# Kernel optimization log

Hardware: AMD Instinct MI355X
Metric: run time of the kernel (lower is better)

## Reference

```python
import jax, jax.numpy as jnp
import numpy as np

N_NODES = 100000
EPS = 1e-5  # BatchNorm1d default eps


def gcn_conv(x, W, b, row, col, n):
    """PyG GCNConv: add self-loops, symmetric normalization, linear, scatter-add."""
    loop = jnp.arange(n, dtype=row.dtype)
    row_f = jnp.concatenate([row, loop])  # sources
    col_f = jnp.concatenate([col, loop])  # targets
    # degree of target nodes (edge_weight = 1)
    deg = jax.ops.segment_sum(jnp.ones_like(col_f, dtype=x.dtype), col_f, num_segments=n)
    dinv = jnp.where(deg > 0, jax.lax.rsqrt(deg), 0.0)
    norm = dinv[row_f] * dinv[col_f]  # [E+N]
    h = x @ W  # [N, out]
    msg = h[row_f] * norm[:, None]  # [E+N, out]
    out = jax.ops.segment_sum(msg, col_f, num_segments=n)
    return out + b


def batch_norm(x, gamma, beta):
    # training-mode BatchNorm1d: biased batch stats over node axis
    mean = jnp.mean(x, axis=0)
    var = jnp.var(x, axis=0)
    return (x - mean) * jax.lax.rsqrt(var + EPS) * gamma + beta


def setup_inputs() -> dict:
    key = jax.random.key(0)
    ks = jax.random.split(key, 8)
    n, e, f_in, h = N_NODES, 1600000, 25, 128
    x = jax.random.normal(ks[0], (n, f_in), dtype=jnp.float32)
    edge_index = jax.random.randint(ks[1], (2, e), 0, n, dtype=jnp.int64)
    s1 = 1.0 / np.sqrt(f_in)
    s2 = 1.0 / np.sqrt(h)
    W1 = jax.random.uniform(ks[2], (f_in, h), jnp.float32, -s1, s1)
    b1 = jax.random.uniform(ks[3], (h,), jnp.float32, -s1, s1)
    gamma = jnp.ones((h,), jnp.float32)
    beta = jnp.zeros((h,), jnp.float32)
    W2 = jax.random.uniform(ks[4], (h, h), jnp.float32, -s2, s2)
    b2 = jax.random.uniform(ks[5], (h,), jnp.float32, -s2, s2)
    return {"x": x, "edge_index": edge_index, "W1": W1, "b1": b1,
            "gamma": gamma, "beta": beta, "W2": W2, "b2": b2}


def reference(x, edge_index, W1, b1, gamma, beta, W2, b2):
    row, col = edge_index[0], edge_index[1]
    n = x.shape[0]
    h = jax.nn.relu(gcn_conv(x, W1, b1, row, col, n))
    h = batch_norm(h, gamma, beta)
    h = jax.nn.relu(gcn_conv(h, W2, b2, row, col, n))
    return h
```

## Files before the change

kernel.cpp:

```cpp
#include <hip/hip_runtime.h>
#include <stdint.h>


#define HID 128
#define NBB 512

typedef short bf16x8 __attribute__((ext_vector_type(8)));
typedef float f32x4 __attribute__((ext_vector_type(4)));

__device__ __forceinline__ unsigned short f2bf(float f) {
    unsigned int u = __float_as_uint(f);
    unsigned int r = (u + 0x7FFFu + ((u >> 16) & 1u)) >> 16;
    return (unsigned short)r;
}
__device__ __forceinline__ unsigned int pack2bf(float lo, float hi) {
    return (unsigned int)f2bf(lo) | ((unsigned int)f2bf(hi) << 16);
}
__device__ __forceinline__ float bflo(unsigned int v) { return __uint_as_float(v << 16); }
__device__ __forceinline__ float bfhi(unsigned int v) { return __uint_as_float(v & 0xffff0000u); }

__global__ void detect_kernel(const unsigned int* __restrict__ w, int* __restrict__ mode, int nwords) {
    __shared__ int any;
    if (threadIdx.x == 0) any = 0;
    __syncthreads();
    for (int i = threadIdx.x * 2 + 1; i < nwords && i < 8192; i += 512) {
        if (w[i] != 0) atomicOr(&any, 1);
    }
    __syncthreads();
    if (threadIdx.x == 0) *mode = any ? 0 : 1;
}

__device__ __forceinline__ int load_idx(const void* ei, size_t i, int mode) {
    return mode ? (int)((const long long*)ei)[i] : ((const int*)ei)[i];
}

__global__ __launch_bounds__(256) void count_q_kernel(const void* __restrict__ ei,
                                                      const int* __restrict__ modep,
                                                      int* __restrict__ qcnt,
                                                      int E, int CHUNK, int nchunk) {
    __shared__ int qc[512];
    for (int i = threadIdx.x; i < nchunk; i += 256) qc[i] = 0;
    __syncthreads();
    int mode = *modep;
    int beg = blockIdx.x * CHUNK;
    int end = beg + CHUNK; if (end > E) end = E;
    for (int e = beg + threadIdx.x; e < end; e += 256) {
        int c = load_idx(ei, (size_t)E + e, mode);
        atomicAdd(&qc[c >> 8], 1);
    }
    __syncthreads();
    for (int i = threadIdx.x; i < nchunk; i += 256)
        qcnt[blockIdx.x * nchunk + i] = qc[i];
}

__global__ __launch_bounds__(256) void scanq_partial_kernel(const int* __restrict__ qcnt,
                                                            int* __restrict__ blocksum,
                                                            int NQ, int nchunk) {
    int j0 = blockIdx.x * 2048 + threadIdx.x * 8;
    int s = 0;
    #pragma unroll
    for (int i = 0; i < 8; ++i) {
        int j = j0 + i;
        if (j < NQ) {
            int q = j >> 9, b = j & (NBB - 1);
            s += qcnt[b * nchunk + q];
        }
    }
    #pragma unroll
    for (int off = 32; off > 0; off >>= 1) s += __shfl_down(s, off);
    __shared__ int ls[4];
    if ((threadIdx.x & 63) == 0) ls[threadIdx.x >> 6] = s;
    __syncthreads();
    if (threadIdx.x == 0) blocksum[blockIdx.x] = ls[0] + ls[1] + ls[2] + ls[3];
}

__global__ __launch_bounds__(1024) void scanq_blocksums_kernel(const int* __restrict__ blocksum,
                                                               int* __restrict__ blockoff,
                                                               int* __restrict__ qoff,
                                                               int nsb, int NQ) {
    __shared__ int s[1024];
    int t = threadIdx.x;
    int own = (t < nsb) ? blocksum[t] : 0;
    s[t] = own;
    __syncthreads();
    for (int off = 1; off < 1024; off <<= 1) {
        int v = s[t] + ((t >= off) ? s[t - off] : 0);
        __syncthreads();
        s[t] = v;
        __syncthreads();
    }
    if (t < nsb) blockoff[t] = s[t] - own;
    if (t == 1023) qoff[NQ] = s[1023];
}

__global__ __launch_bounds__(256) void scanq_finalize_kernel(const int* __restrict__ qcnt,
                                                             const int* __restrict__ blockoff,
                                                             int* __restrict__ qoff,
                                                             int NQ, int nchunk) {
    int t = threadIdx.x;
    int j0 = blockIdx.x * 2048 + t * 8;
    int v[8], own = 0;
    #pragma unroll
    for (int i = 0; i < 8; ++i) {
        int j = j0 + i;
        v[i] = 0;
        if (j < NQ) {
            int q = j >> 9, b = j & (NBB - 1);
            v[i] = qcnt[b * nchunk + q];
        }
        own += v[i];
    }
    __shared__ int s[256];
    s[t] = own;
    __syncthreads();
    for (int off = 1; off < 256; off <<= 1) {
        int x = s[t] + ((t >= off) ? s[t - off] : 0);
        __syncthreads();
        s[t] = x;
        __syncthreads();
    }
    int e = blockoff[blockIdx.x] + s[t] - own;
    #pragma unroll
    for (int i = 0; i < 8; ++i) {
        int j = j0 + i;
        if (j < NQ) qoff[j] = e;
        e += v[i];
    }
}

__global__ __launch_bounds__(256) void bin_kernel(const void* __restrict__ ei,
                                                  const int* __restrict__ modep,
                                                  const int* __restrict__ qoff,
                                                  unsigned int* __restrict__ packed,
                                                  int E, int CHUNK, int nchunk) {
    __shared__ int cur[512];
    for (int i = threadIdx.x; i < nchunk; i += 256)
        cur[i] = qoff[i * NBB + blockIdx.x];
    __syncthreads();
    int mode = *modep;
    int beg = blockIdx.x * CHUNK;
    int end = beg + CHUNK; if (end > E) end = E;
    for (int e = beg + threadIdx.x; e < end; e += 256) {
        int c = load_idx(ei, (size_t)E + e, mode);
        int r = load_idx(ei, (size_t)e, mode);
        int pos = atomicAdd(&cur[c >> 8], 1);
        packed[pos] = ((unsigned)(c & 255) << 24) | (unsigned)r;
    }
}

__global__ __launch_bounds__(256) void chunk_build_kernel(
    const unsigned int* __restrict__ packed, const int* __restrict__ qoff,
    int* __restrict__ rowptr, float* __restrict__ dinv,
    int* __restrict__ edge_src, int n, int E) {
    int q = blockIdx.x;
    int t = threadIdx.x;
    int pbeg = qoff[q * NBB];
    int pend = qoff[(q + 1) * NBB];
    __shared__ int cnt256[256], cur[256], s[256];
    cnt256[t] = 0;
    __syncthreads();
    for (int i = pbeg + t; i < pend; i += 256)
        atomicAdd(&cnt256[packed[i] >> 24], 1);
    __syncthreads();
    int own = cnt256[t];
    s[t] = own;
    __syncthreads();
    for (int off = 1; off < 256; off <<= 1) {
        int x = s[t] + ((t >= off) ? s[t - off] : 0);
        __syncthreads();
        s[t] = x;
        __syncthreads();
    }
    int pref = s[t] - own;
    int node = (q << 8) + t;
    if (node < n) {
        rowptr[node] = pbeg + pref;
        dinv[node] = rsqrtf((float)(own + 1));
    }
    cur[t] = pbeg + pref;
    if (q == gridDim.x - 1 && t == 0) rowptr[n] = E;
    __syncthreads();
    for (int i = pbeg + t; i < pend; i += 256) {
        unsigned int u = packed[i];
        int pos = atomicAdd(&cur[u >> 24], 1);
        edge_src[pos] = (int)(u & 0xFFFFFFu);
    }
}

__global__ __launch_bounds__(256) void gemm1_kernel(const float* __restrict__ x,
                                                    const float* __restrict__ W,
                                                    unsigned short* __restrict__ h, int n) {
    __shared__ float lw[25 * HID];
    for (int i = threadIdx.x; i < 25 * HID; i += 256) lw[i] = W[i];
    __syncthreads();
    int g = threadIdx.x >> 7, c = threadIdx.x & 127;
    for (int r = blockIdx.x * 2 + g; r < n; r += gridDim.x * 2) {
        const float* xr = x + (size_t)r * 25;
        float acc = 0.f;
        #pragma unroll
        for (int k = 0; k < 25; ++k) acc = fmaf(xr[k], lw[k * HID + c], acc);
        h[(size_t)r * HID + c] = f2bf(acc);
    }
}

__global__ __launch_bounds__(256) void propagate_kernel(
    const unsigned short* __restrict__ h, const int* __restrict__ rowptr,
    const int* __restrict__ edge_src, const float* __restrict__ dinv,
    const float* __restrict__ bias, float* __restrict__ out, int n) {
    int wid = (blockIdx.x * 256 + threadIdx.x) >> 6;
    if (wid >= n) return;
    int lane = threadIdx.x & 63;
    int beg = rowptr[wid], end = rowptr[wid + 1];
    float dc = dinv[wid];
    float ax = 0.f, ay = 0.f;
    const unsigned int* hp = (const unsigned int*)h;
    for (int b = beg; b < end; b += 64) {
        int m = end - b; if (m > 64) m = 64;
        int s = 0; float w = 0.f;
        if (lane < m) { s = edge_src[b + lane]; w = dinv[s]; }
        int j = 0;
        for (; j + 8 <= m; j += 8) {
            int s0 = __shfl(s, j + 0), s1 = __shfl(s, j + 1);
            int s2 = __shfl(s, j + 2), s3 = __shfl(s, j + 3);
            int s4 = __shfl(s, j + 4), s5 = __shfl(s, j + 5);
            int s6 = __shfl(s, j + 6), s7 = __shfl(s, j + 7);
            unsigned int v0 = hp[(size_t)s0 * 64 + lane];
            unsigned int v1 = hp[(size_t)s1 * 64 + lane];
            unsigned int v2 = hp[(size_t)s2 * 64 + lane];
            unsigned int v3 = hp[(size_t)s3 * 64 + lane];
            unsigned int v4 = hp[(size_t)s4 * 64 + lane];
            unsigned int v5 = hp[(size_t)s5 * 64 + lane];
            unsigned int v6 = hp[(size_t)s6 * 64 + lane];
            unsigned int v7 = hp[(size_t)s7 * 64 + lane];
            float w0 = __shfl(w, j + 0), w1 = __shfl(w, j + 1);
            float w2 = __shfl(w, j + 2), w3 = __shfl(w, j + 3);
            float w4 = __shfl(w, j + 4), w5 = __shfl(w, j + 5);
            float w6 = __shfl(w, j + 6), w7 = __shfl(w, j + 7);
            ax = fmaf(bflo(v0), w0, ax); ay = fmaf(bfhi(v0), w0, ay);
            ax = fmaf(bflo(v1), w1, ax); ay = fmaf(bfhi(v1), w1, ay);
            ax = fmaf(bflo(v2), w2, ax); ay = fmaf(bfhi(v2), w2, ay);
            ax = fmaf(bflo(v3), w3, ax); ay = fmaf(bfhi(v3), w3, ay);
            ax = fmaf(bflo(v4), w4, ax); ay = fmaf(bfhi(v4), w4, ay);
            ax = fmaf(bflo(v5), w5, ax); ay = fmaf(bfhi(v5), w5, ay);
            ax = fmaf(bflo(v6), w6, ax); ay = fmaf(bfhi(v6), w6, ay);
            ax = fmaf(bflo(v7), w7, ax); ay = fmaf(bfhi(v7), w7, ay);
        }
        for (; j < m; ++j) {
            int sj = __shfl(s, j);
            float wj = __shfl(w, j);
            unsigned int v = hp[(size_t)sj * 64 + lane];
            ax = fmaf(bflo(v), wj, ax);
            ay = fmaf(bfhi(v), wj, ay);
        }
    }
    {
        unsigned int v = hp[(size_t)wid * 64 + lane];
        ax = fmaf(bflo(v), dc, ax);
        ay = fmaf(bfhi(v), dc, ay);
    }
    float bx = bias[lane * 2], by = bias[lane * 2 + 1];
    ax = fmaxf(fmaf(ax, dc, bx), 0.f);
    ay = fmaxf(fmaf(ay, dc, by), 0.f);
    *(float2*)(out + (size_t)wid * HID + lane * 2) = make_float2(ax, ay);
}

__global__ __launch_bounds__(256) void bn_stats_kernel(const float* __restrict__ y,
                                                       float* __restrict__ sum,
                                                       float* __restrict__ sumsq, int n) {
    int c = threadIdx.x & 127;
    int g = threadIdx.x >> 7;
    float s = 0.f, s2 = 0.f;
    for (int r = blockIdx.x * 2 + g; r < n; r += gridDim.x * 2) {
        float v = y[(size_t)r * HID + c];
        s += v;
        s2 = fmaf(v, v, s2);
    }
    __shared__ float ls[256], ls2[256];
    ls[threadIdx.x] = s; ls2[threadIdx.x] = s2;
    __syncthreads();
    if (threadIdx.x < 128) {
        atomicAdd(&sum[c], ls[threadIdx.x] + ls[threadIdx.x + 128]);
        atomicAdd(&sumsq[c], ls2[threadIdx.x] + ls2[threadIdx.x + 128]);
    }
}

__global__ void bn_finalize_kernel(const float* __restrict__ sum, const float* __restrict__ sumsq,
                                   const float* __restrict__ gamma, const float* __restrict__ beta,
                                   float* __restrict__ scale, float* __restrict__ shift, float inv_n) {
    int c = threadIdx.x;
    float mean = sum[c] * inv_n;
    float var = sumsq[c] * inv_n - mean * mean;
    float sc = gamma[c] * rsqrtf(var + 1e-5f);
    scale[c] = sc;
    shift[c] = beta[c] - mean * sc;
}

__global__ __launch_bounds__(256) void wt_kernel(const float* __restrict__ W,
                                                 unsigned short* __restrict__ Wt) {
    int idx = blockIdx.x * 256 + threadIdx.x;
    int c = idx >> 7, k = idx & 127;
    Wt[c * 128 + k] = f2bf(W[k * 128 + c]);
}

__global__ __launch_bounds__(256) void gemm2_mfma_kernel(
    const float* __restrict__ y, const unsigned short* __restrict__ Wt,
    const float* __restrict__ scale, const float* __restrict__ shift,
    unsigned short* __restrict__ out, int n) {
    __shared__ unsigned short lwt[128 * 136];
    __shared__ unsigned short ly[128 * 136];
    int t = threadIdx.x;
    int base = blockIdx.x * 128;

    {
        const unsigned int* w32 = (const unsigned int*)Wt;
        unsigned int* l32 = (unsigned int*)lwt;
        #pragma unroll
        for (int i = 0; i < 32; ++i) {
            int idx = t + i * 256;
            int r = idx >> 6, cp = idx & 63;
            l32[r * 68 + cp] = w32[r * 64 + cp];
        }
    }
    {
        int r = t >> 1, hh = t & 1;
        int gr = base + r;
        unsigned int* l32 = (unsigned int*)ly;
        const float4* yrow = (const float4*)(y + (size_t)gr * HID + hh * 64);
        #pragma unroll
        for (int j = 0; j < 16; ++j) {
            float4 v = make_float4(0.f, 0.f, 0.f, 0.f);
            if (gr < n) v = yrow[j];
            int gk = hh * 64 + j * 4;
            float a0 = fmaf(v.x, scale[gk + 0], shift[gk + 0]);
            float a1 = fmaf(v.y, scale[gk + 1], shift[gk + 1]);
            float a2 = fmaf(v.z, scale[gk + 2], shift[gk + 2]);
            float a3 = fmaf(v.w, scale[gk + 3], shift[gk + 3]);
            l32[r * 68 + hh * 32 + j * 2 + 0] = pack2bf(a0, a1);
            l32[r * 68 + hh * 32 + j * 2 + 1] = pack2bf(a2, a3);
        }
    }
    __syncthreads();

    int w = t >> 6, lane = t & 63;
    int li = lane & 15, lg = lane >> 4;
    f32x4 acc[2][8];
    #pragma unroll
    for (int a = 0; a < 2; ++a)
        #pragma unroll
        for (int b = 0; b < 8; ++b) acc[a][b] = (f32x4){0.f, 0.f, 0.f, 0.f};

    #pragma unroll
    for (int ks = 0; ks < 4; ++ks) {
        int kb = ks * 32 + lg * 8;
        bf16x8 af[2], bfr[8];
        #pragma unroll
        for (int rt = 0; rt < 2; ++rt)
            af[rt] = *(const bf16x8*)&ly[(w * 32 + rt * 16 + li) * 136 + kb];
        #pragma unroll
        for (int cf = 0; cf < 8; ++cf)
            bfr[cf] = *(const bf16x8*)&lwt[(cf * 16 + li) * 136 + kb];
        #pragma unroll
        for (int rt = 0; rt < 2; ++rt)
            #pragma unroll
            for (int cf = 0; cf < 8; ++cf)
                acc[rt][cf] = __builtin_amdgcn_mfma_f32_16x16x32_bf16(
                    af[rt], bfr[cf], acc[rt][cf], 0, 0, 0);
    }

    #pragma unroll
    for (int rt = 0; rt < 2; ++rt) {
        #pragma unroll
        for (int reg = 0; reg < 4; ++reg) {
            int gr = base + w * 32 + rt * 16 + lg * 4 + reg;
            if (gr < n) {
                #pragma unroll
                for (int cf = 0; cf < 8; ++cf)
                    out[(size_t)gr * HID + cf * 16 + li] = f2bf(acc[rt][cf][reg]);
            }
        }
    }
}

extern "C" void kernel_launch(void* const* d_in, const int* in_sizes, int n_in,
                              void* d_out, int out_size, void* d_ws, size_t ws_size,
                              hipStream_t stream) {
    const float* x     = (const float*)d_in[0];
    const void*  ei    = d_in[1];
    const float* W1    = (const float*)d_in[2];
    const float* b1    = (const float*)d_in[3];
    const float* gamma = (const float*)d_in[4];
    const float* beta  = (const float*)d_in[5];
    const float* W2    = (const float*)d_in[6];
    const float* b2    = (const float*)d_in[7];
    float* out = (float*)d_out;

    const int f_in = 25;
    int n = in_sizes[0] / f_in;
    int E = in_sizes[1] / 2;
    int nchunk = (n + 255) >> 8;
    int NQ = nchunk * NBB;
    int nsb = (NQ + 2047) / 2048;
    int CHUNK = (E + NBB - 1) / NBB;

    char* ws = (char*)d_ws;
    size_t off = 0;
    auto alloc = [&](size_t bytes) -> void* {
        void* p = ws + off;
        off += (bytes + 511) & ~(size_t)511;
        return p;
    };
    int*   rowptr    = (int*)alloc(((size_t)n + 1) * 4);
    float* dinv      = (float*)alloc((size_t)n * 4);
    int*   edge_src  = (int*)alloc((size_t)E * 4);
    unsigned int* packed = (unsigned int*)alloc((size_t)E * 4);
    int*   qcnt      = (int*)alloc((size_t)NQ * 4);
    int*   qoff      = (int*)alloc(((size_t)NQ + 1) * 4);
    int*   blocksum  = (int*)alloc((size_t)nsb * 4);
    int*   blockoff  = (int*)alloc((size_t)nsb * 4);
    float* bnacc     = (float*)alloc(256 * 4);
    float* sclshift  = (float*)alloc(256 * 4);
    int*   mode      = (int*)alloc(4);
    unsigned short* Wt = (unsigned short*)alloc(128 * 128 * 2);
    unsigned short* h  = (unsigned short*)alloc((size_t)n * HID * 2);

    hipMemsetAsync(bnacc, 0, 256 * 4, stream);

    detect_kernel<<<1, 256, 0, stream>>>((const unsigned int*)ei, mode, 2 * E);
    count_q_kernel<<<NBB, 256, 0, stream>>>(ei, mode, qcnt, E, CHUNK, nchunk);
    scanq_partial_kernel<<<nsb, 256, 0, stream>>>(qcnt, blocksum, NQ, nchunk);
    scanq_blocksums_kernel<<<1, 1024, 0, stream>>>(blocksum, blockoff, qoff, nsb, NQ);
    scanq_finalize_kernel<<<nsb, 256, 0, stream>>>(qcnt, blockoff, qoff, NQ, nchunk);
    bin_kernel<<<NBB, 256, 0, stream>>>(ei, mode, qoff, packed, E, CHUNK, nchunk);
    chunk_build_kernel<<<nchunk, 256, 0, stream>>>(packed, qoff, rowptr, dinv, edge_src, n, E);

    gemm1_kernel<<<4096, 256, 0, stream>>>(x, W1, h, n);
    propagate_kernel<<<(n + 3) / 4, 256, 0, stream>>>(h, rowptr, edge_src, dinv, b1, out, n);

    bn_stats_kernel<<<512, 256, 0, stream>>>(out, bnacc, bnacc + 128, n);
    bn_finalize_kernel<<<1, 128, 0, stream>>>(bnacc, bnacc + 128, gamma, beta,
                                              sclshift, sclshift + 128, 1.0f / (float)n);

    wt_kernel<<<64, 256, 0, stream>>>(W2, Wt);
    gemm2_mfma_kernel<<<(n + 127) / 128, 256, 0, stream>>>(out, Wt, sclshift, sclshift + 128, h, n);
    propagate_kernel<<<(n + 3) / 4, 256, 0, stream>>>(h, rowptr, edge_src, dinv, b2, out, n);
}
```

Measured before the change: 312.1 us.

## Aggregate raw 25-dim features before first GCN linear layer

Reorders the first GCN layer to propagate the 25-wide input features (padded to 32 bf16) over the graph first, then apply the 25x128 linear, bias and ReLU. The gather traffic per edge drops from 128 bf16 values to 32, which cuts the memory-bound propagation cost of layer one. It adds a padding kernel and two small intermediate buffers. Inputs are also rounded to bf16 before aggregation, a slightly different rounding order from before.

```diff
diff --git a/kernel.cpp b/kernel.cpp
--- a/kernel.cpp
+++ b/kernel.cpp
@@ -187,19 +187,76 @@
     }
 }
 
-__global__ __launch_bounds__(256) void gemm1_kernel(const float* __restrict__ x,
+__global__ __launch_bounds__(256) void xpad_kernel(const float* __restrict__ x,
+                                                   unsigned int* __restrict__ xp, int n) {
+    int r = blockIdx.x * 256 + threadIdx.x;
+    if (r >= n) return;
+    const float* xr = x + (size_t)r * 25;
+    unsigned int* o = xp + (size_t)r * 16;
+    #pragma unroll
+    for (int j = 0; j < 12; ++j)
+        o[j] = pack2bf(xr[j * 2], xr[j * 2 + 1]);
+    o[12] = pack2bf(xr[24], 0.f);
+    o[13] = 0u; o[14] = 0u; o[15] = 0u;
+}
+
+__global__ __launch_bounds__(256) void prop_x_kernel(
+    const unsigned int* __restrict__ xp, const int* __restrict__ rowptr,
+    const int* __restrict__ edge_src, const float* __restrict__ dinv,
+    unsigned int* __restrict__ y0, int n) {
+    int wid = (blockIdx.x * 256 + threadIdx.x) >> 6;
+    if (wid >= n) return;
+    int lane = threadIdx.x & 63;
+    int g = lane >> 4, i = lane & 15;
+    int beg = rowptr[wid], end = rowptr[wid + 1];
+    float dc = dinv[wid];
+    float ax = 0.f, ay = 0.f;
+    for (int b = beg; b < end; b += 64) {
+        int m = end - b; if (m > 64) m = 64;
+        int s = 0; float w = 0.f;
+        if (lane < m) { s = edge_src[b + lane]; w = dinv[s]; }
+        int nsteps = (m + 3) >> 2;
+        for (int t = 0; t < nsteps; ++t) {
+            int e = 4 * t + g;
+            int sj = __shfl(s, e & 63);
+            float wj = __shfl(w, e & 63);
+            if (e >= m) { sj = 0; wj = 0.f; }
+            unsigned int u = xp[(size_t)sj * 16 + i];
+            ax = fmaf(bflo(u), wj, ax);
+            ay = fmaf(bfhi(u), wj, ay);
+        }
+    }
+    if (g == 0) {
+        unsigned int u = xp[(size_t)wid * 16 + i];
+        ax = fmaf(bflo(u), dc, ax);
+        ay = fmaf(bfhi(u), dc, ay);
+    }
+    ax += __shfl_xor(ax, 16); ax += __shfl_xor(ax, 32);
+    ay += __shfl_xor(ay, 16); ay += __shfl_xor(ay, 32);
+    if (lane < 16)
+        y0[(size_t)wid * 16 + i] = pack2bf(ax * dc, ay * dc);
+}
+
+__global__ __launch_bounds__(256) void gemm1_kernel(const unsigned int* __restrict__ y0,
                                                     const float* __restrict__ W,
-                                                    unsigned short* __restrict__ h, int n) {
+                                                    const float* __restrict__ bias,
+                                                    float* __restrict__ y1, int n) {
     __shared__ float lw[25 * HID];
     for (int i = threadIdx.x; i < 25 * HID; i += 256) lw[i] = W[i];
     __syncthreads();
     int g = threadIdx.x >> 7, c = threadIdx.x & 127;
+    float bc = bias[c];
     for (int r = blockIdx.x * 2 + g; r < n; r += gridDim.x * 2) {
-        const float* xr = x + (size_t)r * 25;
-        float acc = 0.f;
-        #pragma unroll
-        for (int k = 0; k < 25; ++k) acc = fmaf(xr[k], lw[k * HID + c], acc);
-        h[(size_t)r * HID + c] = f2bf(acc);
+        const unsigned int* yr = y0 + (size_t)r * 16;
+        float acc = bc;
+        #pragma unroll
+        for (int j = 0; j < 12; ++j) {
+            unsigned int u = yr[j];
+            acc = fmaf(bflo(u), lw[(j * 2 + 0) * HID + c], acc);
+            acc = fmaf(bfhi(u), lw[(j * 2 + 1) * HID + c], acc);
+        }
+        acc = fmaf(bflo(yr[12]), lw[24 * HID + c], acc);
+        y1[(size_t)r * HID + c] = fmaxf(acc, 0.f);
     }
 }
 
@@ -420,6 +477,8 @@
     float* bnacc     = (float*)alloc(256 * 4);
     float* sclshift  = (float*)alloc(256 * 4);
     int*   mode      = (int*)alloc(4);
+    unsigned int* xp  = (unsigned int*)alloc((size_t)n * 16 * 4);
+    unsigned int* y0  = (unsigned int*)alloc((size_t)n * 16 * 4);
     unsigned short* Wt = (unsigned short*)alloc(128 * 128 * 2);
     unsigned short* h  = (unsigned short*)alloc((size_t)n * HID * 2);
 
@@ -433,8 +492,9 @@
     bin_kernel<<<NBB, 256, 0, stream>>>(ei, mode, qoff, packed, E, CHUNK, nchunk);
     chunk_build_kernel<<<nchunk, 256, 0, stream>>>(packed, qoff, rowptr, dinv, edge_src, n, E);
 
-    gemm1_kernel<<<4096, 256, 0, stream>>>(x, W1, h, n);
-    propagate_kernel<<<(n + 3) / 4, 256, 0, stream>>>(h, rowptr, edge_src, dinv, b1, out, n);
+    xpad_kernel<<<(n + 255) / 256, 256, 0, stream>>>(x, xp, n);
+    prop_x_kernel<<<(n + 3) / 4, 256, 0, stream>>>(xp, rowptr, edge_src, dinv, y0, n);
+    gemm1_kernel<<<4096, 256, 0, stream>>>(y0, W1, b1, out, n);
 
     bn_stats_kernel<<<512, 256, 0, stream>>>(out, bnacc, bnacc + 128, n);
     bn_finalize_kernel<<<1, 128, 0, stream>>>(bnacc, bnacc + 128, gamma, beta,
```

Result: faster. 282.4 us (-9.5%).
